# Performance work log

Measured on AMD Instinct MI355X. Metric: run time of the kernel, lower is better.

## Reference

```python
import jax, jax.numpy as jnp
import numpy as np

HIDDEN = 2048
VOCAB = 32768
SEQ = 4608
N_CHUNKS = 9
CAP = 30.0
IGNORE = -100


def setup_inputs() -> dict:
    key = jax.random.key(0)
    k1, k2, k3 = jax.random.split(key, 3)
    weight = (jax.random.normal(k1, (VOCAB, HIDDEN), dtype=jnp.float32) * 0.02).astype(jnp.bfloat16)
    hidden = jax.random.normal(k2, (1, SEQ, HIDDEN), dtype=jnp.float32)
    input_ids = jax.random.randint(k3, (1, SEQ), 0, VOCAB)
    attention_mask = jnp.ones((1, SEQ), dtype=jnp.int32)
    return {"weight": weight, "hidden": hidden, "input_ids": input_ids,
            "attention_mask": attention_mask}


def _build_labels(input_ids, attention_mask):
    # labels[t] = input_ids[t+1], masked-out positions and the final position -> -100
    ids = input_ids[0]
    am = attention_mask[0]
    lab = jnp.where(am[1:] == 0, IGNORE, ids[1:])            # [S-1]
    lab = jnp.concatenate([lab, jnp.full((1,), IGNORE, lab.dtype)])  # [S]
    return lab


def reference(weight, hidden, input_ids, attention_mask):
    labels = _build_labels(input_ids, attention_mask)        # [S]
    x = hidden.reshape(-1, HIDDEN)                           # [S, H] fp32
    chunk = SEQ // N_CHUNKS
    xs = x.reshape(N_CHUNKS, chunk, HIDDEN)
    ls = labels.reshape(N_CHUNKS, chunk)

    wT = weight.T                                            # [H, V] bf16

    def chunk_loss(args):
        xc, lc = args                                        # [c,H], [c]
        # softcapped logits: CAP * tanh((x @ W^T) / CAP), mm in bf16
        t = jnp.tanh((xc.astype(jnp.bfloat16) @ wT) / CAP).astype(jnp.float32)  # [c,V]
        z = CAP * (t - jnp.max(t, axis=1, keepdims=True))    # stable shifted logits
        logp = z - jnp.log(jnp.sum(jnp.exp(z), axis=1, keepdims=True))
        valid = lc != IGNORE
        idx = jnp.where(valid, lc, 0)
        nll = -jnp.take_along_axis(logp, idx[:, None], axis=1)[:, 0]
        return jnp.sum(jnp.where(valid, nll, 0.0))

    losses = jax.lax.map(chunk_loss, (xs, ls))               # [N_CHUNKS]
    return jnp.sum(losses)
```

## Files before the change

### kernel.cpp

```cpp
#include <hip/hip_runtime.h>
#include <hip/hip_bf16.h>
#include <cstdint>

#define S_LEN   4608
#define HID     2048
#define VOCAB_N 32768
#define CAPV    30.0f
#define IGNORE_IDX (-100)
#define NT512   512

typedef short bf16x8 __attribute__((ext_vector_type(8)));
typedef float f32x4  __attribute__((ext_vector_type(4)));

__device__ __forceinline__ unsigned short f2bf_rtne(float f) {
    unsigned int u = __float_as_uint(f);
    unsigned int r = u + 0x7fffu + ((u >> 16) & 1u);
    return (unsigned short)(r >> 16);
}
__device__ __forceinline__ float bfr(float f) {
    unsigned int u = __float_as_uint(f);
    unsigned int r = u + 0x7fffu + ((u >> 16) & 1u);
    return __uint_as_float(r & 0xffff0000u);
}
__device__ __forceinline__ float bf_lo(unsigned int u) { return __uint_as_float(u << 16); }
__device__ __forceinline__ float bf_hi(unsigned int u) { return __uint_as_float(u & 0xffff0000u); }
__device__ __forceinline__ float bfdot2(unsigned int x, unsigned int w) {
    return bf_lo(x) * bf_lo(w) + bf_hi(x) * bf_hi(w);
}
__device__ __forceinline__ float softcap_ref(float logit) {
    float lb = bfr(logit);
    float x  = bfr(lb / CAPV);
    float e  = __expf(2.0f * x);
    float t  = bfr((e - 1.0f) / (e + 1.0f));
    return CAPV * t;
}

__global__ void cvt_kernel(const float* __restrict__ h, unsigned short* __restrict__ xb) {
    int i = blockIdx.x * blockDim.x + threadIdx.x;
    float4 v = ((const float4*)h)[i];
    ushort4 o;
    o.x = f2bf_rtne(v.x); o.y = f2bf_rtne(v.y);
    o.z = f2bf_rtne(v.z); o.w = f2bf_rtne(v.w);
    ((ushort4*)xb)[i] = o;
}

__global__ __launch_bounds__(256)
void gemm_lse_kernel(const unsigned short* __restrict__ X,
                     const unsigned short* __restrict__ W,
                     float* __restrict__ partL) {
    __shared__ __align__(16) unsigned short As[128 * 64];
    __shared__ __align__(16) unsigned short Bs[128 * 64];

    const int tid  = threadIdx.x;
    const int wave = tid >> 6;
    const int lane = tid & 63;
    const int tileM = blockIdx.y * 128;
    const int tileN = blockIdx.x * 128;

    const int r8 = lane >> 3;
    const int s8 = lane & 7;
    const int cg = s8 ^ r8;

    const unsigned short* Abase = X + (size_t)(tileM + wave * 32) * HID + cg * 8;
    const unsigned short* Bbase = W + (size_t)(tileN + wave * 32) * HID + cg * 8;

    const int wr  = wave >> 1, wc = wave & 1;
    const int q   = lane >> 4, l16 = lane & 15;

    const int c0 = ((q)     ^ (l16 & 7)) * 8;
    const int c1 = ((4 | q) ^ (l16 & 7)) * 8;
    int arow[4], brow[4];
    #pragma unroll
    for (int t = 0; t < 4; ++t) {
        arow[t] = (wr * 64 + t * 16 + l16) * 64;
        brow[t] = (wc * 64 + t * 16 + l16) * 64;
    }

    f32x4 acc[4][4] = {};

    for (int k0 = 0; k0 < HID; k0 += 64) {
        __syncthreads();
        #pragma unroll
        for (int j = 0; j < 4; ++j) {
            const unsigned short* ga = Abase + (size_t)(j * 8 + r8) * HID + k0;
            __builtin_amdgcn_global_load_lds(
                (const __attribute__((address_space(1))) void*)ga,
                (__attribute__((address_space(3))) void*)&As[(wave * 32 + j * 8) * 64],
                16, 0, 0);
            const unsigned short* gb = Bbase + (size_t)(j * 8 + r8) * HID + k0;
            __builtin_amdgcn_global_load_lds(
                (const __attribute__((address_space(1))) void*)gb,
                (__attribute__((address_space(3))) void*)&Bs[(wave * 32 + j * 8) * 64],
                16, 0, 0);
        }
        __syncthreads();

        #pragma unroll
        for (int kk = 0; kk < 2; ++kk) {
            const int cs = kk ? c1 : c0;
            bf16x8 av[4], bv[4];
            #pragma unroll
            for (int t = 0; t < 4; ++t) {
                av[t] = *(const bf16x8*)&As[arow[t] + cs];
                bv[t] = *(const bf16x8*)&Bs[brow[t] + cs];
            }
            #pragma unroll
            for (int ti = 0; ti < 4; ++ti)
                #pragma unroll
                for (int tj = 0; tj < 4; ++tj)
                    acc[ti][tj] = __builtin_amdgcn_mfma_f32_16x16x32_bf16(
                        av[ti], bv[tj], acc[ti][tj], 0, 0, 0);
        }
    }

    const int rowbase = tileM + wr * 64;
    const int ntile   = blockIdx.x * 2 + wc;
    #pragma unroll
    for (int ti = 0; ti < 4; ++ti) {
        #pragma unroll
        for (int r = 0; r < 4; ++r) {
            float s = 0.0f;
            #pragma unroll
            for (int tj = 0; tj < 4; ++tj)
                s += __expf(softcap_ref(acc[ti][tj][r]));
            s += __shfl_xor(s, 1);
            s += __shfl_xor(s, 2);
            s += __shfl_xor(s, 4);
            s += __shfl_xor(s, 8);
            if (l16 == 0)
                partL[(size_t)(rowbase + ti * 16 + q * 4 + r) * NT512 + ntile] = s;
        }
    }
}

__global__ void row_reduce_kernel(const unsigned short* __restrict__ X,
                                  const unsigned short* __restrict__ W,
                                  const int* __restrict__ ids,
                                  const int* __restrict__ am,
                                  const float* __restrict__ partL,
                                  float* __restrict__ out) {
    __shared__ float blk[4];
    const int wave = threadIdx.x >> 6;
    const int lane = threadIdx.x & 63;
    const int r = blockIdx.x * 4 + wave;

    int lab = IGNORE_IDX;
    if (r < S_LEN - 1 && am[r + 1] != 0) lab = ids[r + 1];
    const bool valid = (lab >= 0 && lab < VOCAB_N);

    float dot = 0.0f;
    if (valid) {
        const unsigned short* xr = X + (size_t)r   * HID;
        const unsigned short* wr = W + (size_t)lab * HID;
        #pragma unroll
        for (int c = 0; c < 4; ++c) {
            const int off = c * 512 + lane * 8;
            uint4 xu = *(const uint4*)(xr + off);
            uint4 wu = *(const uint4*)(wr + off);
            dot += bfdot2(xu.x, wu.x) + bfdot2(xu.y, wu.y) +
                   bfdot2(xu.z, wu.z) + bfdot2(xu.w, wu.w);
        }
    }
    #pragma unroll
    for (int m = 1; m < 64; m <<= 1) dot += __shfl_xor(dot, m);

    float L = 0.0f;
    const float* pr = partL + (size_t)r * NT512;
    #pragma unroll
    for (int i = 0; i < 8; ++i) L += pr[i * 64 + lane];
    #pragma unroll
    for (int m = 1; m < 64; m <<= 1) L += __shfl_xor(L, m);

    if (lane == 0) {
        float loss = 0.0f;
        if (valid) loss = logf(L) - softcap_ref(dot);
        blk[wave] = loss;
    }
    __syncthreads();
    if (threadIdx.x == 0)
        atomicAdd(out, blk[0] + blk[1] + blk[2] + blk[3]);
}

extern "C" void kernel_launch(void* const* d_in, const int* in_sizes, int n_in,
                              void* d_out, int out_size, void* d_ws, size_t ws_size,
                              hipStream_t stream) {
    const unsigned short* W  = (const unsigned short*)d_in[0];
    const float*  hidden     = (const float*)d_in[1];
    const int*    ids        = (const int*)d_in[2];
    const int*    am         = (const int*)d_in[3];
    float* out = (float*)d_out;

    char* ws = (char*)d_ws;
    unsigned short* Xb = (unsigned short*)ws;
    float* partL       = (float*)(ws + (size_t)S_LEN * HID * 2);

    hipMemsetAsync(out, 0, (size_t)out_size * 4, stream);

    cvt_kernel<<<(S_LEN * HID / 4) / 256, 256, 0, stream>>>(hidden, Xb);

    dim3 g(VOCAB_N / 128, S_LEN / 128);
    gemm_lse_kernel<<<g, 256, 0, stream>>>(Xb, W, partL);

    row_reduce_kernel<<<S_LEN / 4, 256, 0, stream>>>(Xb, W, ids, am, partL, out);
}
```

Baseline: 1.208 ms.

## Run vocab GEMM in FP8 e4m3 using scaled MFMA

Converts the activations (scaled by 32) and the weights (scaled by 256) to FP8 e4m3 in a single fused conversion kernel. The main GEMM then uses the 16x16x128 f8f6f4 scaled MFMA with K-step 128, and the accumulator is rescaled by 1/8192 before the softcap. The memset is folded into the conversion kernel. This aims to double MFMA throughput and halve GEMM operand traffic, but adds a pass over the full weight matrix on every call and loses precision in the logsumexp, which may break tolerance.

```diff
diff --git a/kernel.cpp b/kernel.cpp
--- a/kernel.cpp
+++ b/kernel.cpp
@@ -8,9 +8,11 @@
 #define CAPV    30.0f
 #define IGNORE_IDX (-100)
 #define NT512   512
+#define XBLK    4608
 
 typedef short bf16x8 __attribute__((ext_vector_type(8)));
 typedef float f32x4  __attribute__((ext_vector_type(4)));
+typedef int   i32x8  __attribute__((ext_vector_type(8)));
 
 __device__ __forceinline__ unsigned short f2bf_rtne(float f) {
     unsigned int u = __float_as_uint(f);
@@ -22,6 +24,7 @@
     unsigned int r = u + 0x7fffu + ((u >> 16) & 1u);
     return __uint_as_float(r & 0xffff0000u);
 }
+__device__ __forceinline__ float bf2f(unsigned int us) { return __uint_as_float(us << 16); }
 __device__ __forceinline__ float bf_lo(unsigned int u) { return __uint_as_float(u << 16); }
 __device__ __forceinline__ float bf_hi(unsigned int u) { return __uint_as_float(u & 0xffff0000u); }
 __device__ __forceinline__ float bfdot2(unsigned int x, unsigned int w) {
@@ -34,22 +37,74 @@
     float t  = bfr((e - 1.0f) / (e + 1.0f));
     return CAPV * t;
 }
-
-__global__ void cvt_kernel(const float* __restrict__ h, unsigned short* __restrict__ xb) {
-    int i = blockIdx.x * blockDim.x + threadIdx.x;
-    float4 v = ((const float4*)h)[i];
-    ushort4 o;
-    o.x = f2bf_rtne(v.x); o.y = f2bf_rtne(v.y);
-    o.z = f2bf_rtne(v.z); o.w = f2bf_rtne(v.w);
-    ((ushort4*)xb)[i] = o;
+__device__ __forceinline__ unsigned int f2e4m3(float x) {
+    unsigned int u = __float_as_uint(x);
+    unsigned int s = (u >> 24) & 0x80u;
+    unsigned int a = u & 0x7fffffffu;
+    unsigned int m;
+    if (a >= 0x43e00000u) {
+        m = 0x7eu;
+    } else if (a < 0x3c800000u) {
+        m = (unsigned int)__float2int_rn(__uint_as_float(a) * 512.0f);
+    } else {
+        unsigned int r = a + 0x7ffffu + ((a >> 20) & 1u);
+        m = (r >> 20) - 960u;
+    }
+    return s | m;
+}
+
+__global__ void cvt_kernel(const float* __restrict__ h,
+                           const unsigned short* __restrict__ W,
+                           unsigned short* __restrict__ Xb,
+                           unsigned char* __restrict__ Xf8,
+                           unsigned char* __restrict__ Wf8,
+                           float* __restrict__ out) {
+    const int bid = blockIdx.x;
+    const int t   = threadIdx.x;
+    if (bid == 0 && t == 0) out[0] = 0.0f;
+    if (bid < XBLK) {
+        const size_t i = ((size_t)bid * 256 + t) * 8;
+        float4 v0 = *(const float4*)(h + i);
+        float4 v1 = *(const float4*)(h + i + 4);
+        unsigned short b[8];
+        b[0] = f2bf_rtne(v0.x); b[1] = f2bf_rtne(v0.y);
+        b[2] = f2bf_rtne(v0.z); b[3] = f2bf_rtne(v0.w);
+        b[4] = f2bf_rtne(v1.x); b[5] = f2bf_rtne(v1.y);
+        b[6] = f2bf_rtne(v1.z); b[7] = f2bf_rtne(v1.w);
+        ushort4 o0 = {b[0], b[1], b[2], b[3]};
+        ushort4 o1 = {b[4], b[5], b[6], b[7]};
+        *(ushort4*)(Xb + i)     = o0;
+        *(ushort4*)(Xb + i + 4) = o1;
+        unsigned int p0 = 0, p1 = 0;
+        #pragma unroll
+        for (int j = 0; j < 4; ++j) p0 |= f2e4m3(bf2f(b[j])     * 32.0f) << (8 * j);
+        #pragma unroll
+        for (int j = 0; j < 4; ++j) p1 |= f2e4m3(bf2f(b[4 + j]) * 32.0f) << (8 * j);
+        uint2 p = {p0, p1};
+        *(uint2*)(Xf8 + i) = p;
+    } else {
+        const size_t i = ((size_t)(bid - XBLK) * 256 + t) * 8;
+        uint4 w = *(const uint4*)(W + i);
+        unsigned int p0 = 0, p1 = 0;
+        p0 |= f2e4m3(bf_lo(w.x) * 256.0f);
+        p0 |= f2e4m3(bf_hi(w.x) * 256.0f) << 8;
+        p0 |= f2e4m3(bf_lo(w.y) * 256.0f) << 16;
+        p0 |= f2e4m3(bf_hi(w.y) * 256.0f) << 24;
+        p1 |= f2e4m3(bf_lo(w.z) * 256.0f);
+        p1 |= f2e4m3(bf_hi(w.z) * 256.0f) << 8;
+        p1 |= f2e4m3(bf_lo(w.w) * 256.0f) << 16;
+        p1 |= f2e4m3(bf_hi(w.w) * 256.0f) << 24;
+        uint2 p = {p0, p1};
+        *(uint2*)(Wf8 + i) = p;
+    }
 }
 
 __global__ __launch_bounds__(256)
-void gemm_lse_kernel(const unsigned short* __restrict__ X,
-                     const unsigned short* __restrict__ W,
+void gemm_lse_kernel(const unsigned char* __restrict__ Xf8,
+                     const unsigned char* __restrict__ Wf8,
                      float* __restrict__ partL) {
-    __shared__ __align__(16) unsigned short As[128 * 64];
-    __shared__ __align__(16) unsigned short Bs[128 * 64];
+    __shared__ __align__(16) unsigned char As[128 * 128];
+    __shared__ __align__(16) unsigned char Bs[128 * 128];
 
     const int tid  = threadIdx.x;
     const int wave = tid >> 6;
@@ -57,59 +112,66 @@
     const int tileM = blockIdx.y * 128;
     const int tileN = blockIdx.x * 128;
 
-    const int r8 = lane >> 3;
-    const int s8 = lane & 7;
-    const int cg = s8 ^ r8;
-
-    const unsigned short* Abase = X + (size_t)(tileM + wave * 32) * HID + cg * 8;
-    const unsigned short* Bbase = W + (size_t)(tileN + wave * 32) * HID + cg * 8;
-
-    const int wr  = wave >> 1, wc = wave & 1;
-    const int q   = lane >> 4, l16 = lane & 15;
-
-    const int c0 = ((q)     ^ (l16 & 7)) * 8;
-    const int c1 = ((4 | q) ^ (l16 & 7)) * 8;
+    const int rr = lane >> 3;
+    const int sl = lane & 7;
+    const int cg = sl ^ rr;
+
+    const unsigned char* Abase = Xf8 + (size_t)(tileM + wave * 32) * HID + cg * 16;
+    const unsigned char* Bbase = Wf8 + (size_t)(tileN + wave * 32) * HID + cg * 16;
+
+    const int wr = wave >> 1, wc = wave & 1;
+    const int q  = lane >> 4, l16 = lane & 15;
+
+    const int sA0 = ((q)     ^ (l16 & 7)) * 16;
+    const int sA1 = ((q + 4) ^ (l16 & 7)) * 16;
     int arow[4], brow[4];
     #pragma unroll
     for (int t = 0; t < 4; ++t) {
-        arow[t] = (wr * 64 + t * 16 + l16) * 64;
-        brow[t] = (wc * 64 + t * 16 + l16) * 64;
+        arow[t] = (wr * 64 + t * 16 + l16) * 128;
+        brow[t] = (wc * 64 + t * 16 + l16) * 128;
     }
 
     f32x4 acc[4][4] = {};
 
-    for (int k0 = 0; k0 < HID; k0 += 64) {
+    for (int k0 = 0; k0 < HID; k0 += 128) {
         __syncthreads();
         #pragma unroll
         for (int j = 0; j < 4; ++j) {
-            const unsigned short* ga = Abase + (size_t)(j * 8 + r8) * HID + k0;
+            const unsigned char* ga = Abase + (size_t)(j * 8 + rr) * HID + k0;
             __builtin_amdgcn_global_load_lds(
                 (const __attribute__((address_space(1))) void*)ga,
-                (__attribute__((address_space(3))) void*)&As[(wave * 32 + j * 8) * 64],
+                (__attribute__((address_space(3))) void*)&As[(wave * 32 + j * 8) * 128],
                 16, 0, 0);
-            const unsigned short* gb = Bbase + (size_t)(j * 8 + r8) * HID + k0;
+            const unsigned char* gb = Bbase + (size_t)(j * 8 + rr) * HID + k0;
             __builtin_amdgcn_global_load_lds(
                 (const __attribute__((address_space(1))) void*)gb,
-                (__attribute__((address_space(3))) void*)&Bs[(wave * 32 + j * 8) * 64],
+                (__attribute__((address_space(3))) void*)&Bs[(wave * 32 + j * 8) * 128],
                 16, 0, 0);
         }
         __syncthreads();
 
-        #pragma unroll
-        for (int kk = 0; kk < 2; ++kk) {
-            const int cs = kk ? c1 : c0;
-            bf16x8 av[4], bv[4];
-            #pragma unroll
-            for (int t = 0; t < 4; ++t) {
-                av[t] = *(const bf16x8*)&As[arow[t] + cs];
-                bv[t] = *(const bf16x8*)&Bs[brow[t] + cs];
-            }
+        union U8 { uint4 u4[2]; i32x8 v; };
+        i32x8 av[4];
+        #pragma unroll
+        for (int t = 0; t < 4; ++t) {
+            U8 u;
+            u.u4[0] = *(const uint4*)&As[arow[t] + sA0];
+            u.u4[1] = *(const uint4*)&As[arow[t] + sA1];
+            av[t] = u.v;
+        }
+        #pragma unroll
+        for (int tj = 0; tj < 4; ++tj) {
+            U8 u;
+            u.u4[0] = *(const uint4*)&Bs[brow[tj] + sA0];
+            u.u4[1] = *(const uint4*)&Bs[brow[tj] + sA1];
+            i32x8 bv = u.v;
             #pragma unroll
             for (int ti = 0; ti < 4; ++ti)
-                #pragma unroll
-                for (int tj = 0; tj < 4; ++tj)
-                    acc[ti][tj] = __builtin_amdgcn_mfma_f32_16x16x32_bf16(
-                        av[ti], bv[tj], acc[ti][tj], 0, 0, 0);
+                acc[ti][tj] = __builtin_amdgcn_mfma_scale_f32_16x16x128_f8f6f4(
+                    av[ti], bv, acc[ti][tj],
+                    0, 0,
+                    0, 0x7f7f7f7f,
+                    0, 0x7f7f7f7f);
         }
     }
 
@@ -122,7 +184,7 @@
             float s = 0.0f;
             #pragma unroll
             for (int tj = 0; tj < 4; ++tj)
-                s += __expf(softcap_ref(acc[ti][tj][r]));
+                s += __expf(softcap_ref(acc[ti][tj][r] * (1.0f / 8192.0f)));
             s += __shfl_xor(s, 1);
             s += __shfl_xor(s, 2);
             s += __shfl_xor(s, 4);
@@ -191,15 +253,17 @@
     float* out = (float*)d_out;
 
     char* ws = (char*)d_ws;
-    unsigned short* Xb = (unsigned short*)ws;
-    float* partL       = (float*)(ws + (size_t)S_LEN * HID * 2);
-
-    hipMemsetAsync(out, 0, (size_t)out_size * 4, stream);
-
-    cvt_kernel<<<(S_LEN * HID / 4) / 256, 256, 0, stream>>>(hidden, Xb);
+    unsigned short* Xb  = (unsigned short*)ws;
+    float* partL        = (float*)(ws + (size_t)S_LEN * HID * 2);
+    unsigned char* Xf8  = (unsigned char*)(ws + (size_t)S_LEN * HID * 2
+                                              + (size_t)S_LEN * NT512 * 4);
+    unsigned char* Wf8  = Xf8 + (size_t)S_LEN * HID;
+
+    cvt_kernel<<<XBLK + (VOCAB_N * HID / 2048), 256, 0, stream>>>(
+        hidden, W, Xb, Xf8, Wf8, out);
 
     dim3 g(VOCAB_N / 128, S_LEN / 128);
-    gemm_lse_kernel<<<g, 256, 0, stream>>>(Xb, W, partL);
+    gemm_lse_kernel<<<g, 256, 0, stream>>>(Xf8, Wf8, partL);
 
     row_reduce_kernel<<<S_LEN / 4, 256, 0, stream>>>(Xb, W, ids, am, partL, out);
 }
```

Result: slower. 1.304 ms (+7.9%).

## Halve GEMM K-tile to 32, swap grid axes, fold output zeroing into convert kernel

Applied to the files above, without the earlier changes.

Shrinks the per-iteration K slab from 64 to 32, which halves LDS use per block (16KB instead of 32KB) and uses a new XOR swizzle for the 32-wide rows. It also drops the launch bounds and swaps the grid so the M tiles vary fastest, meaning consecutive blocks share the same weight tile for L2 reuse. The output memset is removed and out[0] is zeroed inside the convert kernel instead, saving one API call. In exchange there are twice as many barriers and loop iterations per K, and each sync has less MFMA work to hide it.

```diff
diff --git a/kernel.cpp b/kernel.cpp
--- a/kernel.cpp
+++ b/kernel.cpp
@@ -35,7 +35,9 @@
     return CAPV * t;
 }
 
-__global__ void cvt_kernel(const float* __restrict__ h, unsigned short* __restrict__ xb) {
+__global__ void cvt_kernel(const float* __restrict__ h, unsigned short* __restrict__ xb,
+                           float* __restrict__ out) {
+    if (blockIdx.x == 0 && threadIdx.x == 0) out[0] = 0.0f;
     int i = blockIdx.x * blockDim.x + threadIdx.x;
     float4 v = ((const float4*)h)[i];
     ushort4 o;
@@ -44,22 +46,20 @@
     ((ushort4*)xb)[i] = o;
 }
 
-__global__ __launch_bounds__(256)
-void gemm_lse_kernel(const unsigned short* __restrict__ X,
-                     const unsigned short* __restrict__ W,
-                     float* __restrict__ partL) {
-    __shared__ __align__(16) unsigned short As[128 * 64];
-    __shared__ __align__(16) unsigned short Bs[128 * 64];
+__global__ void gemm_lse_kernel(const unsigned short* __restrict__ X,
+                                const unsigned short* __restrict__ W,
+                                float* __restrict__ partL) {
+    __shared__ __align__(16) unsigned short As[128 * 32];
+    __shared__ __align__(16) unsigned short Bs[128 * 32];
 
     const int tid  = threadIdx.x;
     const int wave = tid >> 6;
     const int lane = tid & 63;
-    const int tileM = blockIdx.y * 128;
-    const int tileN = blockIdx.x * 128;
+    const int tileM = blockIdx.x * 128;
+    const int tileN = blockIdx.y * 128;
 
-    const int r8 = lane >> 3;
-    const int s8 = lane & 7;
-    const int cg = s8 ^ r8;
+    const int lr = lane >> 2;
+    const int cg = (lane & 3) ^ ((lane >> 4) & 3);
 
     const unsigned short* Abase = X + (size_t)(tileM + wave * 32) * HID + cg * 8;
     const unsigned short* Bbase = W + (size_t)(tileN + wave * 32) * HID + cg * 8;
@@ -67,54 +67,49 @@
     const int wr  = wave >> 1, wc = wave & 1;
     const int q   = lane >> 4, l16 = lane & 15;
 
-    const int c0 = ((q)     ^ (l16 & 7)) * 8;
-    const int c1 = ((4 | q) ^ (l16 & 7)) * 8;
+    const int swz = (q ^ (l16 >> 2)) * 8;
     int arow[4], brow[4];
     #pragma unroll
     for (int t = 0; t < 4; ++t) {
-        arow[t] = (wr * 64 + t * 16 + l16) * 64;
-        brow[t] = (wc * 64 + t * 16 + l16) * 64;
+        arow[t] = (wr * 64 + t * 16 + l16) * 32 + swz;
+        brow[t] = (wc * 64 + t * 16 + l16) * 32 + swz;
     }
 
     f32x4 acc[4][4] = {};
 
-    for (int k0 = 0; k0 < HID; k0 += 64) {
+    for (int k0 = 0; k0 < HID; k0 += 32) {
         __syncthreads();
         #pragma unroll
-        for (int j = 0; j < 4; ++j) {
-            const unsigned short* ga = Abase + (size_t)(j * 8 + r8) * HID + k0;
+        for (int j = 0; j < 2; ++j) {
+            const unsigned short* ga = Abase + (size_t)(j * 16 + lr) * HID + k0;
             __builtin_amdgcn_global_load_lds(
                 (const __attribute__((address_space(1))) void*)ga,
-                (__attribute__((address_space(3))) void*)&As[(wave * 32 + j * 8) * 64],
+                (__attribute__((address_space(3))) void*)&As[(wave * 32 + j * 16) * 32],
                 16, 0, 0);
-            const unsigned short* gb = Bbase + (size_t)(j * 8 + r8) * HID + k0;
+            const unsigned short* gb = Bbase + (size_t)(j * 16 + lr) * HID + k0;
             __builtin_amdgcn_global_load_lds(
                 (const __attribute__((address_space(1))) void*)gb,
-                (__attribute__((address_space(3))) void*)&Bs[(wave * 32 + j * 8) * 64],
+                (__attribute__((address_space(3))) void*)&Bs[(wave * 32 + j * 16) * 32],
                 16, 0, 0);
         }
         __syncthreads();
 
+        bf16x8 av[4], bv[4];
         #pragma unroll
-        for (int kk = 0; kk < 2; ++kk) {
-            const int cs = kk ? c1 : c0;
-            bf16x8 av[4], bv[4];
+        for (int t = 0; t < 4; ++t) {
+            av[t] = *(const bf16x8*)&As[arow[t]];
+            bv[t] = *(const bf16x8*)&Bs[brow[t]];
+        }
+        #pragma unroll
+        for (int ti = 0; ti < 4; ++ti)
             #pragma unroll
-            for (int t = 0; t < 4; ++t) {
-                av[t] = *(const bf16x8*)&As[arow[t] + cs];
-                bv[t] = *(const bf16x8*)&Bs[brow[t] + cs];
-            }
-            #pragma unroll
-            for (int ti = 0; ti < 4; ++ti)
-                #pragma unroll
-                for (int tj = 0; tj < 4; ++tj)
-                    acc[ti][tj] = __builtin_amdgcn_mfma_f32_16x16x32_bf16(
-                        av[ti], bv[tj], acc[ti][tj], 0, 0, 0);
-        }
+            for (int tj = 0; tj < 4; ++tj)
+                acc[ti][tj] = __builtin_amdgcn_mfma_f32_16x16x32_bf16(
+                    av[ti], bv[tj], acc[ti][tj], 0, 0, 0);
     }
 
     const int rowbase = tileM + wr * 64;
-    const int ntile   = blockIdx.x * 2 + wc;
+    const int ntile   = blockIdx.y * 2 + wc;
     #pragma unroll
     for (int ti = 0; ti < 4; ++ti) {
         #pragma unroll
@@ -194,11 +189,9 @@
     unsigned short* Xb = (unsigned short*)ws;
     float* partL       = (float*)(ws + (size_t)S_LEN * HID * 2);
 
-    hipMemsetAsync(out, 0, (size_t)out_size * 4, stream);
+    cvt_kernel<<<(S_LEN * HID / 4) / 256, 256, 0, stream>>>(hidden, Xb, out);
 
-    cvt_kernel<<<(S_LEN * HID / 4) / 256, 256, 0, stream>>>(hidden, Xb);
-
-    dim3 g(VOCAB_N / 128, S_LEN / 128);
+    dim3 g(S_LEN / 128, VOCAB_N / 128);
     gemm_lse_kernel<<<g, 256, 0, stream>>>(Xb, W, partL);
 
     row_reduce_kernel<<<S_LEN / 4, 256, 0, stream>>>(Xb, W, ids, am, partL, out);
```

Result: faster. 1.032 ms (-14.6%).
